# Kernel optimization log

Measured on AMD Instinct MI355X. Metric: run time of the kernel, lower is better.

The kernel has to match this reference:

```python
import jax, jax.numpy as jnp
import numpy as np


def _init_relative_position_index(window_size: int) -> np.ndarray:
    coords = np.stack(np.meshgrid(np.arange(window_size), np.arange(window_size), indexing='ij'))
    coords_flatten = coords.reshape(2, -1)  # [2, wh*ww]
    rel = coords_flatten[:, :, None] - coords_flatten[:, None, :]  # [2, N, N]
    rel = rel.transpose(1, 2, 0).copy()
    rel[:, :, 0] += window_size - 1
    rel[:, :, 1] += window_size - 1
    rel[:, :, 0] *= 2 * window_size - 1
    return rel.sum(-1)  # [N, N] int


def setup_inputs() -> dict:
    B_, N, C, H, WH, NW = 2048, 49, 512, 16, 7, 64
    key = jax.random.key(0)
    ks = jax.random.split(key, 6)
    x = jax.random.normal(ks[0], (B_, N, C), dtype=jnp.float32)
    qkv_w = jax.random.normal(ks[1], (3 * C, C), dtype=jnp.float32) * 0.02
    qkv_b = jax.random.normal(ks[2], (3 * C,), dtype=jnp.float32) * 0.02
    rp_bias_table = jax.random.normal(ks[3], ((2 * WH - 1) ** 2, H), dtype=jnp.float32) * 0.02
    out_w = jax.random.normal(ks[4], (C, C), dtype=jnp.float32) * 0.02
    out_b = jax.random.normal(ks[5], (C,), dtype=jnp.float32) * 0.02
    rp_index = jnp.asarray(_init_relative_position_index(WH), dtype=jnp.int32)
    mask = jnp.zeros((NW, N, N), dtype=jnp.float32)  # 0/-inf shifted-window mask
    return {"x": x, "qkv_w": qkv_w, "qkv_b": qkv_b, "rp_index": rp_index,
            "rp_bias_table": rp_bias_table, "out_w": out_w, "out_b": out_b,
            "mask": mask, "nw": NW}


def reference(x, qkv_w, qkv_b, rp_index, rp_bias_table, out_w, out_b, mask, nw):
    B_, N, C = x.shape
    h = rp_bias_table.shape[1]
    dh = C // h
    scale = float(dh) ** -0.5

    # QKV projection; weight layout is (h dh 3) x C per the module's note.
    qkv = x @ qkv_w.T + qkv_b                      # [B_, N, 3C]
    qkv = qkv.reshape(B_, N, h, dh, 3)             # [B_, N, h, dh, 3]
    q = qkv[..., 0].transpose(0, 2, 1, 3)          # [B_, h, N, dh]
    k = qkv[..., 1].transpose(0, 2, 1, 3)
    v = qkv[..., 2].transpose(0, 2, 1, 3)

    attn = jnp.einsum('bhnd,bhmd->bhnm', q * scale, k)  # [B_, h, N, N]

    # gather relative position bias: [N*N] -> [N, N, h] -> [h, N, N]
    pb = rp_bias_table[rp_index.reshape(-1)].reshape(N, N, h).transpose(2, 0, 1)
    # NOTE: original adds the bias TWICE (attn += pb; attn += pb[None]); replicate.
    attn = attn + pb[None]
    attn = attn + pb[None]

    nW = mask.shape[0]
    attn = attn.reshape(B_ // nW, nW, h, N, N) + mask[None, :, None]
    attn = attn.reshape(B_, h, N, N)
    attn = jax.nn.softmax(attn, axis=-1)
    # attn_drop = proj_drop = 0.0 -> dropout is identity

    out = jnp.einsum('bhnm,bhmd->bhnd', attn, v)   # [B_, h, N, dh]
    out = out.transpose(0, 2, 1, 3).reshape(B_, N, h * dh)
    out = out @ out_w.T + out_b
    return out
```

## Files before the change

kernel.cpp:

```cpp
#include <hip/hip_runtime.h>
#include <hip/hip_bf16.h>
#include <stdint.h>

typedef short s16x8 __attribute__((ext_vector_type(8)));
typedef float f32x4 __attribute__((ext_vector_type(4)));

#define H_ 16
#define DH 32
#define NTOK 49
#define CDIM 512
#define SCALE 0.17677669529663687f

typedef const __attribute__((address_space(1))) uint32_t* gas_ptr;
typedef __attribute__((address_space(3))) uint32_t* las_ptr;
#define GLL16(g, l) __builtin_amdgcn_global_load_lds((gas_ptr)(g), (las_ptr)(l), 16, 0, 0)

__device__ __forceinline__ short f2bf(float f){
  union { float f; uint32_t u; } v; v.f = f;
  uint32_t r = v.u + 0x7fffu + ((v.u >> 16) & 1u);
  return (short)(r >> 16);
}

__device__ __forceinline__ s16x8 pack8(float4 a, float4 b){
  s16x8 r;
  r[0]=f2bf(a.x); r[1]=f2bf(a.y); r[2]=f2bf(a.z); r[3]=f2bf(a.w);
  r[4]=f2bf(b.x); r[5]=f2bf(b.y); r[6]=f2bf(b.z); r[7]=f2bf(b.w);
  return r;
}

__global__ void prep_wq_kernel(const float* __restrict__ w, const float* __restrict__ b,
                               short* __restrict__ wq, float* __restrict__ pb)
{
  int t = blockIdx.x*256 + threadIdx.x;
  int jp = t >> 6, kg = t & 63;
  int s = jp >> 9, h = (jp >> 5) & 15, d = jp & 31;
  int srow = h*96 + d*3 + s;
  float fac = (s == 0) ? SCALE : 1.0f;
  const float* wr = w + (size_t)srow*CDIM + kg*8;
  float4 a = *(const float4*)wr;
  float4 c = *(const float4*)(wr+4);
  a.x*=fac; a.y*=fac; a.z*=fac; a.w*=fac;
  c.x*=fac; c.y*=fac; c.z*=fac; c.w*=fac;
  ((s16x8*)(wq + (size_t)jp*CDIM))[kg] = pack8(a,c);
  if (kg == 0) pb[jp] = b[srow]*fac;
}

__global__ void prep_wo_kernel(const float* __restrict__ w, short* __restrict__ wo)
{
  int t = blockIdx.x*256 + threadIdx.x;
  int j = t >> 6, kg = t & 63;
  const float* wr = w + (size_t)j*CDIM + kg*8;
  float4 a = *(const float4*)wr;
  float4 c = *(const float4*)(wr+4);
  ((s16x8*)(wo + (size_t)j*CDIM))[kg] = pack8(a,c);
}

__global__ void bias2_kernel(const int* __restrict__ idx, const float* __restrict__ tab,
                             float* __restrict__ b2)
{
  int i = blockIdx.x*256 + threadIdx.x;
  if (i < H_*2401){
    int h = i / 2401, rc = i - h*2401;
    b2[i] = 2.0f * tab[idx[rc]*H_ + h];
  }
}

__global__ void cvt_kernel(const float* __restrict__ src, short* __restrict__ dst, int n8)
{
  int i = blockIdx.x*blockDim.x + threadIdx.x;
  int stride = gridDim.x*blockDim.x;
  for (; i < n8; i += stride){
    float4 a = ((const float4*)src)[2*i];
    float4 b = ((const float4*)src)[2*i+1];
    ((s16x8*)dst)[i] = pack8(a,b);
  }
}

template<int EPI>
__global__ __launch_bounds__(256)
void gemm128(const short* __restrict__ A, const short* __restrict__ Bm,
             const float* __restrict__ pb,
             short* __restrict__ Q, short* __restrict__ Kd, short* __restrict__ V,
             float* __restrict__ outF, int ntiles, int b0)
{
  __shared__ __align__(16) short As[128*64];
  __shared__ __align__(16) short Bs[128*64];
  const int tid = threadIdx.x, w = tid >> 6, l = tid & 63;
  const int mt = blockIdx.x / ntiles, jt = blockIdx.x % ntiles;
  const int wr = w >> 1, wc = w & 1, lg = l >> 4, lc = l & 15;

  const int srow = w*8 + (l >> 3);
  const int kb = (l & 7) * 16;
  const char* ga = (const char*)A  + ((size_t)(mt*128 + srow))*1024 + kb;
  const char* gb = (const char*)Bm + ((size_t)(jt*128 + srow))*1024 + kb;

  f32x4 acc[4][4];
  #pragma unroll
  for (int i=0;i<4;++i)
    #pragma unroll
    for (int j=0;j<4;++j) acc[i][j] = (f32x4){0.f,0.f,0.f,0.f};

  for (int kt=0; kt<8; ++kt){
    const char* gak = ga + kt*128;
    const char* gbk = gb + kt*128;
    #pragma unroll
    for (int i=0;i<4;++i){
      GLL16(gak + i*32768, As + i*2048 + w*512);
      GLL16(gbk + i*32768, Bs + i*2048 + w*512);
    }
    __syncthreads();
    #pragma unroll
    for (int kk=0; kk<2; ++kk){
      s16x8 af[4], bf_[4];
      #pragma unroll
      for (int i=0;i<4;++i) af[i]  = *(const s16x8*)&As[(wr*64 + i*16 + lc)*64 + kk*32 + lg*8];
      #pragma unroll
      for (int j=0;j<4;++j) bf_[j] = *(const s16x8*)&Bs[(wc*64 + j*16 + lc)*64 + kk*32 + lg*8];
      #pragma unroll
      for (int i=0;i<4;++i)
        #pragma unroll
        for (int j=0;j<4;++j)
          acc[i][j] = __builtin_amdgcn_mfma_f32_16x16x32_bf16(af[i], bf_[j], acc[i][j], 0,0,0);
    }
    __syncthreads();
  }

  const int cb = jt*128 + wc*64;
  if (EPI == 0){
    const int s_sel = cb >> 9;
    short* dst = (s_sel==0) ? Q : (s_sel==1 ? Kd : V);
    float bv[4]; int hj[4], dj[4];
    #pragma unroll
    for (int j=0;j<4;++j){
      int cc = cb + j*16 + lc;
      bv[j] = pb[cc];
      hj[j] = (cc >> 5) & 15;
      dj[j] = cc & 31;
    }
    #pragma unroll
    for (int i=0;i<4;++i){
      #pragma unroll
      for (int r=0;r<4;++r){
        int grow = mt*128 + wr*64 + i*16 + lg*4 + r;
        int bl = grow / 49;
        int n  = grow - bl*49;
        #pragma unroll
        for (int j=0;j<4;++j)
          dst[(((size_t)bl*H_ + hj[j])*NTOK + n)*DH + dj[j]] = f2bf(acc[i][j][r] + bv[j]);
      }
    }
  } else {
    float bv[4];
    #pragma unroll
    for (int j=0;j<4;++j) bv[j] = pb[cb + j*16 + lc];
    #pragma unroll
    for (int i=0;i<4;++i){
      #pragma unroll
      for (int r=0;r<4;++r){
        int grow = mt*128 + wr*64 + i*16 + lg*4 + r;
        size_t o = ((size_t)(b0*NTOK) + grow)*CDIM + cb;
        #pragma unroll
        for (int j=0;j<4;++j)
          outF[o + j*16 + lc] = acc[i][j][r] + bv[j];
      }
    }
  }
}

__global__ __launch_bounds__(256)
void attn_kernel(const short* __restrict__ Q, const short* __restrict__ Kt,
                 const short* __restrict__ V, const float* __restrict__ bias2,
                 const float* __restrict__ mask, short* __restrict__ AO,
                 int b0, int nW)
{
  __shared__ __align__(16) short P[4][64][72];
  const int tid = threadIdx.x, wv = tid >> 6, lane = tid & 63;
  const int lg = lane >> 4, lc = lane & 15;
  const int pair = blockIdx.x*4 + wv;
  const int bl = pair >> 4, h = pair & 15;
  const short* q = Q  + ((size_t)bl*H_ + h)*NTOK*DH;
  const short* k = Kt + ((size_t)bl*H_ + h)*NTOK*DH;
  const short* v = V  + ((size_t)bl*H_ + h)*NTOK*DH;

  s16x8 qa[4], kb[4];
  #pragma unroll
  for (int t=0;t<4;++t){
    int r = t*16 + lc; if (r > 48) r = 48;
    qa[t] = *(const s16x8*)(q + r*DH + lg*8);
    kb[t] = *(const s16x8*)(k + r*DH + lg*8);
  }
  f32x4 S[4][4];
  #pragma unroll
  for (int i=0;i<4;++i)
    #pragma unroll
    for (int j=0;j<4;++j) S[i][j] = (f32x4){0.f,0.f,0.f,0.f};
  #pragma unroll
  for (int i=0;i<4;++i)
    #pragma unroll
    for (int j=0;j<4;++j)
      S[i][j] = __builtin_amdgcn_mfma_f32_16x16x32_bf16(qa[i], kb[j], S[i][j], 0,0,0);

  const float* bb = bias2 + (size_t)h*2401;
  const float* mm = mask + (size_t)((b0 + bl) % nW)*2401;

  float rinv[4][4];
  #pragma unroll
  for (int i=0;i<4;++i){
    #pragma unroll
    for (int r=0;r<4;++r){
      int row = i*16 + lg*4 + r;
      float mx = -3.0e38f;
      #pragma unroll
      for (int j=0;j<4;++j){
        int col = j*16 + lc;
        float sv = S[i][j][r];
        if (row < 49 && col < 49) sv += bb[row*49+col] + mm[row*49+col];
        else sv = -1.0e30f;
        S[i][j][r] = sv;
        mx = fmaxf(mx, sv);
      }
      #pragma unroll
      for (int off=1; off<16; off<<=1) mx = fmaxf(mx, __shfl_xor(mx, off, 64));
      float sum = 0.f;
      #pragma unroll
      for (int j=0;j<4;++j){
        float e = __expf(S[i][j][r] - mx);
        S[i][j][r] = e;
        sum += e;
      }
      #pragma unroll
      for (int off=1; off<16; off<<=1) sum += __shfl_xor(sum, off, 64);
      rinv[i][r] = 1.0f / sum;
    }
  }

  #pragma unroll
  for (int i=0;i<4;++i)
    #pragma unroll
    for (int j=0;j<4;++j)
      #pragma unroll
      for (int r=0;r<4;++r)
        P[wv][i*16 + lg*4 + r][j*16 + lc] = f2bf(S[i][j][r]);

  s16x8 vb[2][2];
  #pragma unroll
  for (int kt=0;kt<2;++kt)
    #pragma unroll
    for (int nt=0;nt<2;++nt){
      s16x8 t;
      #pragma unroll
      for (int e=0;e<8;++e){
        int kk = kt*32 + lg*8 + e; if (kk > 48) kk = 48;
        t[e] = v[kk*DH + nt*16 + lc];
      }
      vb[kt][nt] = t;
    }
  f32x4 O[4][2];
  #pragma unroll
  for (int i=0;i<4;++i){ O[i][0] = (f32x4){0.f,0.f,0.f,0.f}; O[i][1] = (f32x4){0.f,0.f,0.f,0.f}; }
  #pragma unroll
  for (int i=0;i<4;++i){
    #pragma unroll
    for (int kt=0;kt<2;++kt){
      s16x8 pa = *(const s16x8*)&P[wv][i*16 + lc][kt*32 + lg*8];
      #pragma unroll
      for (int nt=0;nt<2;++nt)
        O[i][nt] = __builtin_amdgcn_mfma_f32_16x16x32_bf16(pa, vb[kt][nt], O[i][nt], 0,0,0);
    }
  }
  #pragma unroll
  for (int i=0;i<4;++i)
    #pragma unroll
    for (int r=0;r<4;++r){
      int row = i*16 + lg*4 + r;
      if (row < 49){
        size_t o = ((size_t)bl*NTOK + row)*CDIM + h*DH;
        float rv = rinv[i][r];
        AO[o + lc]      = f2bf(O[i][0][r]*rv);
        AO[o + 16 + lc] = f2bf(O[i][1][r]*rv);
      }
    }
}

extern "C" void kernel_launch(void* const* d_in, const int* in_sizes, int n_in,
                              void* d_out, int out_size, void* d_ws, size_t ws_size,
                              hipStream_t stream)
{
  const float* x      = (const float*)d_in[0];
  const float* qkv_w  = (const float*)d_in[1];
  const float* qkv_b  = (const float*)d_in[2];
  const int*   rp_idx = (const int*)d_in[3];
  const float* rp_tab = (const float*)d_in[4];
  const float* out_w  = (const float*)d_in[5];
  const float* out_b  = (const float*)d_in[6];
  const float* mask   = (const float*)d_in[7];
  const int nW = in_sizes[7] / (NTOK*NTOK);
  float* out = (float*)d_out;

  char* base = (char*)d_ws;
  size_t off = 0;
  auto alloc = [&](size_t bytes)->char*{
    char* p = base + off;
    off = (off + bytes + 255) & ~(size_t)255;
    return p;
  };
  float* b2  = (float*)alloc((size_t)H_*2401*4);
  short* wq  = (short*)alloc((size_t)1536*CDIM*2);
  float* pbq = (float*)alloc(1536*4);
  short* wo  = (short*)alloc((size_t)CDIM*CDIM*2);

  int CB = 512;
  while (CB > 128){
    size_t need = off + 5*(size_t)CB*50176;
    if (need <= ws_size) break;
    CB >>= 1;
  }
  short* xb = (short*)alloc((size_t)CB*50176);
  short* Q  = (short*)alloc((size_t)CB*50176);
  short* K  = (short*)alloc((size_t)CB*50176);
  short* V  = (short*)alloc((size_t)CB*50176);
  short* AO = (short*)alloc((size_t)CB*50176);

  hipLaunchKernelGGL(bias2_kernel, dim3((H_*2401 + 255)/256), dim3(256), 0, stream,
                     rp_idx, rp_tab, b2);
  hipLaunchKernelGGL(prep_wq_kernel, dim3(1536*64/256), dim3(256), 0, stream,
                     qkv_w, qkv_b, wq, pbq);
  hipLaunchKernelGGL(prep_wo_kernel, dim3(512*64/256), dim3(256), 0, stream,
                     out_w, wo);

  const int nchunk = 2048 / CB;
  const int mtiles = CB*NTOK/128;
  const int n8 = CB*3136;
  for (int c=0; c<nchunk; ++c){
    int b0 = c*CB;
    hipLaunchKernelGGL(cvt_kernel, dim3(2048), dim3(256), 0, stream,
                       x + (size_t)b0*NTOK*CDIM, xb, n8);
    hipLaunchKernelGGL((gemm128<0>), dim3(mtiles*12), dim3(256), 0, stream,
                       xb, wq, pbq, Q, K, V, (float*)nullptr, 12, b0);
    hipLaunchKernelGGL(attn_kernel, dim3(CB*4), dim3(256), 0, stream,
                       Q, K, V, b2, mask, AO, b0, nW);
    hipLaunchKernelGGL((gemm128<1>), dim3(mtiles*4), dim3(256), 0, stream,
                       AO, wo, out_b, (short*)nullptr, (short*)nullptr, (short*)nullptr,
                       out, 4, b0);
  }
}
```

Before: 605.2 us.

## Use 256x256 double-buffered swizzled GEMM tiles and premerge bias with mask

Replaces the 128x128 single-buffered GEMM with a 256x256 tile and 512 threads. It double-buffers LDS loads with XOR-swizzled layout, interleaves MFMA phases with async global-to-LDS prefetch, raises wave priority around the MFMA phases, and remaps blocks across XCDs. It also precomputes the combined relative-position bias and window mask per (window, head), so attention reads one array instead of two. The intent is better data reuse, hidden load latency and fewer LDS bank conflicts. In exchange it uses 128KB of LDS per block, creates fewer blocks, and adds a larger bias buffer of nW*H*2401 floats.

```diff
diff --git a/kernel.cpp b/kernel.cpp
--- a/kernel.cpp
+++ b/kernel.cpp
@@ -26,6 +26,12 @@
   r[0]=f2bf(a.x); r[1]=f2bf(a.y); r[2]=f2bf(a.z); r[3]=f2bf(a.w);
   r[4]=f2bf(b.x); r[5]=f2bf(b.y); r[6]=f2bf(b.z); r[7]=f2bf(b.w);
   return r;
+}
+
+__device__ __forceinline__ int xcd_swz(int orig, int nwg){
+  int q = nwg >> 3, r = nwg & 7;
+  int x = orig & 7, idx = orig >> 3;
+  return (x < r ? x*(q+1) : r*(q+1) + (x - r)*q) + idx;
 }
 
 __global__ void prep_wq_kernel(const float* __restrict__ w, const float* __restrict__ b,
@@ -55,14 +61,15 @@
   ((s16x8*)(wo + (size_t)j*CDIM))[kg] = pack8(a,c);
 }
 
-__global__ void bias2_kernel(const int* __restrict__ idx, const float* __restrict__ tab,
-                             float* __restrict__ b2)
-{
-  int i = blockIdx.x*256 + threadIdx.x;
-  if (i < H_*2401){
-    int h = i / 2401, rc = i - h*2401;
-    b2[i] = 2.0f * tab[idx[rc]*H_ + h];
-  }
+__global__ void prep_bm_kernel(const int* __restrict__ idx, const float* __restrict__ tab,
+                               const float* __restrict__ mask, float* __restrict__ bm)
+{
+  int wh = blockIdx.x;
+  int w = wh >> 4, h = wh & 15;
+  const float* mw = mask + (size_t)w*2401;
+  float* o = bm + (size_t)wh*2401;
+  for (int i = threadIdx.x; i < 2401; i += 256)
+    o[i] = mw[i] + 2.0f*tab[idx[i]*H_ + h];
 }
 
 __global__ void cvt_kernel(const float* __restrict__ src, short* __restrict__ dst, int n8)
@@ -77,55 +84,142 @@
 }
 
 template<int EPI>
-__global__ __launch_bounds__(256)
-void gemm128(const short* __restrict__ A, const short* __restrict__ Bm,
+__global__ __launch_bounds__(512, 2)
+void gemm256(const short* __restrict__ A, const short* __restrict__ Bm,
              const float* __restrict__ pb,
              short* __restrict__ Q, short* __restrict__ Kd, short* __restrict__ V,
-             float* __restrict__ outF, int ntiles, int b0)
-{
-  __shared__ __align__(16) short As[128*64];
-  __shared__ __align__(16) short Bs[128*64];
+             float* __restrict__ outF, int ntiles, int nwg, int b0)
+{
+  __shared__ __align__(16) char LB[131072];
   const int tid = threadIdx.x, w = tid >> 6, l = tid & 63;
-  const int mt = blockIdx.x / ntiles, jt = blockIdx.x % ntiles;
-  const int wr = w >> 1, wc = w & 1, lg = l >> 4, lc = l & 15;
-
-  const int srow = w*8 + (l >> 3);
-  const int kb = (l & 7) * 16;
-  const char* ga = (const char*)A  + ((size_t)(mt*128 + srow))*1024 + kb;
-  const char* gb = (const char*)Bm + ((size_t)(jt*128 + srow))*1024 + kb;
-
-  f32x4 acc[4][4];
-  #pragma unroll
-  for (int i=0;i<4;++i)
+  const int wg = xcd_swz(blockIdx.x, nwg);
+  const int mt = wg / ntiles, jt = wg % ntiles;
+  const int wr = w >> 2, wc = w & 3;
+  const int lg = l >> 4, lc = l & 15;
+  const int sw = (lc & 7) << 4;
+
+  const int rr = tid >> 3;
+  const int cswz = ((tid & 7) << 4) ^ ((rr & 7) << 4);
+  const char* gA0 = (const char*)A  + ((size_t)(mt*256 + rr))*1024 + cswz;
+  const char* gB0 = (const char*)Bm + ((size_t)(jt*256 + rr))*1024 + cswz;
+
+  f32x4 acc[8][4];
+  #pragma unroll
+  for (int i=0;i<8;++i)
     #pragma unroll
     for (int j=0;j<4;++j) acc[i][j] = (f32x4){0.f,0.f,0.f,0.f};
 
-  for (int kt=0; kt<8; ++kt){
-    const char* gak = ga + kt*128;
-    const char* gbk = gb + kt*128;
-    #pragma unroll
-    for (int i=0;i<4;++i){
-      GLL16(gak + i*32768, As + i*2048 + w*512);
-      GLL16(gbk + i*32768, Bs + i*2048 + w*512);
-    }
-    __syncthreads();
-    #pragma unroll
-    for (int kk=0; kk<2; ++kk){
-      s16x8 af[4], bf_[4];
-      #pragma unroll
-      for (int i=0;i<4;++i) af[i]  = *(const s16x8*)&As[(wr*64 + i*16 + lc)*64 + kk*32 + lg*8];
-      #pragma unroll
-      for (int j=0;j<4;++j) bf_[j] = *(const s16x8*)&Bs[(wc*64 + j*16 + lc)*64 + kk*32 + lg*8];
+  #pragma unroll
+  for (int tt=0; tt<2; ++tt){
+    char* dA = LB + tt*32768;
+    char* dB = LB + 65536 + tt*32768;
+    const int ko = tt*128;
+    GLL16(gA0 + ko,          dA + w*1024);
+    GLL16(gA0 + ko + 65536,  dA + 8192  + w*1024);
+    GLL16(gA0 + ko + 131072, dA + 16384 + w*1024);
+    GLL16(gA0 + ko + 196608, dA + 24576 + w*1024);
+    GLL16(gB0 + ko,          dB + w*1024);
+    GLL16(gB0 + ko + 65536,  dB + 8192  + w*1024);
+    GLL16(gB0 + ko + 131072, dB + 16384 + w*1024);
+    GLL16(gB0 + ko + 196608, dB + 24576 + w*1024);
+  }
+  asm volatile("s_waitcnt vmcnt(8)" ::: "memory");
+  __syncthreads();
+
+  for (int t=0; t<8; ++t){
+    const char* pA = LB + (t&1)*32768 + wr*16384;
+    const char* pB = LB + 65536 + (t&1)*32768 + (wc>>1)*16384;
+    char* dA = LB + (t&1)*32768;
+    char* dB = LB + 65536 + (t&1)*32768;
+    const int ko = (t+2)*128;
+    const int rB = (wc & 1) << 6;
+
+    s16x8 a03[4][2], a47[4][2], b01[2][2], b23[2][2];
+
+    #pragma unroll
+    for (int i=0;i<4;++i)
+      #pragma unroll
+      for (int kk=0;kk<2;++kk)
+        a03[i][kk] = *(const s16x8*)(pA + ((i*16+lc)<<7) + (((kk<<6)+(lg<<4)) ^ sw));
+    #pragma unroll
+    for (int j=0;j<2;++j)
+      #pragma unroll
+      for (int kk=0;kk<2;++kk)
+        b01[j][kk] = *(const s16x8*)(pB + ((rB + j*16+lc)<<7) + (((kk<<6)+(lg<<4)) ^ sw));
+    __syncthreads();
+    __builtin_amdgcn_s_setprio(1);
+    #pragma unroll
+    for (int kk=0;kk<2;++kk)
       #pragma unroll
       for (int i=0;i<4;++i)
         #pragma unroll
-        for (int j=0;j<4;++j)
-          acc[i][j] = __builtin_amdgcn_mfma_f32_16x16x32_bf16(af[i], bf_[j], acc[i][j], 0,0,0);
-    }
-    __syncthreads();
-  }
-
-  const int cb = jt*128 + wc*64;
+        for (int j=0;j<2;++j)
+          acc[i][j] = __builtin_amdgcn_mfma_f32_16x16x32_bf16(a03[i][kk], b01[j][kk], acc[i][j],0,0,0);
+    __builtin_amdgcn_s_setprio(0);
+    __syncthreads();
+
+    #pragma unroll
+    for (int i=0;i<4;++i)
+      #pragma unroll
+      for (int kk=0;kk<2;++kk)
+        a47[i][kk] = *(const s16x8*)(pA + (((i+4)*16+lc)<<7) + (((kk<<6)+(lg<<4)) ^ sw));
+    __syncthreads();
+    __builtin_amdgcn_s_setprio(1);
+    #pragma unroll
+    for (int kk=0;kk<2;++kk)
+      #pragma unroll
+      for (int i=0;i<4;++i)
+        #pragma unroll
+        for (int j=0;j<2;++j)
+          acc[4+i][j] = __builtin_amdgcn_mfma_f32_16x16x32_bf16(a47[i][kk], b01[j][kk], acc[4+i][j],0,0,0);
+    __builtin_amdgcn_s_setprio(0);
+    __syncthreads();
+
+    #pragma unroll
+    for (int j=0;j<2;++j)
+      #pragma unroll
+      for (int kk=0;kk<2;++kk)
+        b23[j][kk] = *(const s16x8*)(pB + ((rB + (j+2)*16+lc)<<7) + (((kk<<6)+(lg<<4)) ^ sw));
+    if (t < 6){
+      GLL16(gA0 + ko,          dA + w*1024);
+      GLL16(gA0 + ko + 65536,  dA + 8192  + w*1024);
+    }
+    __syncthreads();
+    __builtin_amdgcn_s_setprio(1);
+    #pragma unroll
+    for (int kk=0;kk<2;++kk)
+      #pragma unroll
+      for (int i=0;i<4;++i)
+        #pragma unroll
+        for (int j=0;j<2;++j)
+          acc[i][2+j] = __builtin_amdgcn_mfma_f32_16x16x32_bf16(a03[i][kk], b23[j][kk], acc[i][2+j],0,0,0);
+    __builtin_amdgcn_s_setprio(0);
+    __syncthreads();
+
+    if (t < 6){
+      GLL16(gA0 + ko + 131072, dA + 16384 + w*1024);
+      GLL16(gA0 + ko + 196608, dA + 24576 + w*1024);
+      GLL16(gB0 + ko,          dB + w*1024);
+      GLL16(gB0 + ko + 65536,  dB + 8192  + w*1024);
+      GLL16(gB0 + ko + 131072, dB + 16384 + w*1024);
+      GLL16(gB0 + ko + 196608, dB + 24576 + w*1024);
+    }
+    __syncthreads();
+    __builtin_amdgcn_s_setprio(1);
+    #pragma unroll
+    for (int kk=0;kk<2;++kk)
+      #pragma unroll
+      for (int i=0;i<4;++i)
+        #pragma unroll
+        for (int j=0;j<2;++j)
+          acc[4+i][2+j] = __builtin_amdgcn_mfma_f32_16x16x32_bf16(a47[i][kk], b23[j][kk], acc[4+i][2+j],0,0,0);
+    __builtin_amdgcn_s_setprio(0);
+    if (t < 6){ asm volatile("s_waitcnt vmcnt(8)" ::: "memory"); }
+    else      { asm volatile("s_waitcnt vmcnt(0)" ::: "memory"); }
+    __syncthreads();
+  }
+
+  const int cb = jt*256 + wc*64;
   if (EPI == 0){
     const int s_sel = cb >> 9;
     short* dst = (s_sel==0) ? Q : (s_sel==1 ? Kd : V);
@@ -138,10 +232,10 @@
       dj[j] = cc & 31;
     }
     #pragma unroll
-    for (int i=0;i<4;++i){
+    for (int i=0;i<8;++i){
       #pragma unroll
       for (int r=0;r<4;++r){
-        int grow = mt*128 + wr*64 + i*16 + lg*4 + r;
+        int grow = mt*256 + wr*128 + i*16 + lg*4 + r;
         int bl = grow / 49;
         int n  = grow - bl*49;
         #pragma unroll
@@ -154,10 +248,10 @@
     #pragma unroll
     for (int j=0;j<4;++j) bv[j] = pb[cb + j*16 + lc];
     #pragma unroll
-    for (int i=0;i<4;++i){
+    for (int i=0;i<8;++i){
       #pragma unroll
       for (int r=0;r<4;++r){
-        int grow = mt*128 + wr*64 + i*16 + lg*4 + r;
+        int grow = mt*256 + wr*128 + i*16 + lg*4 + r;
         size_t o = ((size_t)(b0*NTOK) + grow)*CDIM + cb;
         #pragma unroll
         for (int j=0;j<4;++j)
@@ -169,9 +263,8 @@
 
 __global__ __launch_bounds__(256)
 void attn_kernel(const short* __restrict__ Q, const short* __restrict__ Kt,
-                 const short* __restrict__ V, const float* __restrict__ bias2,
-                 const float* __restrict__ mask, short* __restrict__ AO,
-                 int b0, int nW)
+                 const short* __restrict__ V, const float* __restrict__ bm,
+                 short* __restrict__ AO, int b0, int nW)
 {
   __shared__ __align__(16) short P[4][64][72];
   const int tid = threadIdx.x, wv = tid >> 6, lane = tid & 63;
@@ -200,8 +293,8 @@
     for (int j=0;j<4;++j)
       S[i][j] = __builtin_amdgcn_mfma_f32_16x16x32_bf16(qa[i], kb[j], S[i][j], 0,0,0);
 
-  const float* bb = bias2 + (size_t)h*2401;
-  const float* mm = mask + (size_t)((b0 + bl) % nW)*2401;
+  const int widx = (b0 + bl) % nW;
+  const float* bmh = bm + ((size_t)widx*H_ + h)*2401;
 
   float rinv[4][4];
   #pragma unroll
@@ -214,7 +307,7 @@
       for (int j=0;j<4;++j){
         int col = j*16 + lc;
         float sv = S[i][j][r];
-        if (row < 49 && col < 49) sv += bb[row*49+col] + mm[row*49+col];
+        if (row < 49 && col < 49) sv += bmh[row*49+col];
         else sv = -1.0e30f;
         S[i][j][r] = sv;
         mx = fmaxf(mx, sv);
@@ -304,7 +397,7 @@
     off = (off + bytes + 255) & ~(size_t)255;
     return p;
   };
-  float* b2  = (float*)alloc((size_t)H_*2401*4);
+  float* bm  = (float*)alloc((size_t)nW*H_*2401*4);
   short* wq  = (short*)alloc((size_t)1536*CDIM*2);
   float* pbq = (float*)alloc(1536*4);
   short* wo  = (short*)alloc((size_t)CDIM*CDIM*2);
@@ -321,26 +414,26 @@
   short* V  = (short*)alloc((size_t)CB*50176);
   short* AO = (short*)alloc((size_t)CB*50176);
 
-  hipLaunchKernelGGL(bias2_kernel, dim3((H_*2401 + 255)/256), dim3(256), 0, stream,
-                     rp_idx, rp_tab, b2);
+  hipLaunchKernelGGL(prep_bm_kernel, dim3(nW*H_), dim3(256), 0, stream,
+                     rp_idx, rp_tab, mask, bm);
   hipLaunchKernelGGL(prep_wq_kernel, dim3(1536*64/256), dim3(256), 0, stream,
                      qkv_w, qkv_b, wq, pbq);
   hipLaunchKernelGGL(prep_wo_kernel, dim3(512*64/256), dim3(256), 0, stream,
                      out_w, wo);
 
   const int nchunk = 2048 / CB;
-  const int mtiles = CB*NTOK/128;
+  const int mtiles = CB*NTOK/256;
   const int n8 = CB*3136;
   for (int c=0; c<nchunk; ++c){
     int b0 = c*CB;
     hipLaunchKernelGGL(cvt_kernel, dim3(2048), dim3(256), 0, stream,
                        x + (size_t)b0*NTOK*CDIM, xb, n8);
-    hipLaunchKernelGGL((gemm128<0>), dim3(mtiles*12), dim3(256), 0, stream,
-                       xb, wq, pbq, Q, K, V, (float*)nullptr, 12, b0);
+    hipLaunchKernelGGL((gemm256<0>), dim3(mtiles*6), dim3(512), 0, stream,
+                       xb, wq, pbq, Q, K, V, (float*)nullptr, 6, mtiles*6, b0);
     hipLaunchKernelGGL(attn_kernel, dim3(CB*4), dim3(256), 0, stream,
-                       Q, K, V, b2, mask, AO, b0, nW);
-    hipLaunchKernelGGL((gemm128<1>), dim3(mtiles*4), dim3(256), 0, stream,
+                       Q, K, V, bm, AO, b0, nW);
+    hipLaunchKernelGGL((gemm256<1>), dim3(mtiles*2), dim3(512), 0, stream,
                        AO, wo, out_b, (short*)nullptr, (short*)nullptr, (short*)nullptr,
-                       out, 4, b0);
-  }
-}
+                       out, 2, mtiles*2, b0);
+  }
+}
```

After: 643.2 us. 6.3% more time.
